# Kernel tuning notes

Hardware: AMD Instinct MI355X
Metric: run time of the kernel (lower is better)

The kernel has to match this reference:

```python
import jax, jax.numpy as jnp
import numpy as np

NUM_CHANNEL = 2                      # channels per telescope group
K = 7                                # hexagonal kernel size
N_LEV = [2048, 512, 128, 32, 8]      # pixels per level (stride-2 hex pooling ~ /4)
CHS = [2, 64, 128, 256, 512]         # channel progression n1->n_features->n2->n3->n4


def _iconv(x, idx, w, b):
    # x: [B,C,Nin], idx: [K,Nout], w: [O,C,K] -> [B,O,Nout]
    g = x[:, :, idx]                              # gather neighbours [B,C,K,Nout]
    return jnp.einsum('bckn,ock->bon', g, w) + b[None, :, None]


def _ipool(x, idx):
    # IndexedMaxPool2d: gather then max over kernel positions
    return x[:, :, idx].max(axis=2)               # [B,C,Nout]


def _bn(x, gamma, beta, eps=1e-5):
    # train-mode BatchNorm1d over (batch, pixel) dims, biased variance (torch semantics)
    m = x.mean(axis=(0, 2), keepdims=True)
    v = x.var(axis=(0, 2), keepdims=True)
    return (x - m) / jnp.sqrt(v + eps) * gamma[None, :, None] + beta[None, :, None]


def setup_inputs() -> dict:
    key = jax.random.key(0)
    ks = jax.random.split(key, 40)
    ki = iter(range(40))
    nk = lambda: ks[next(ki)]
    B = 256
    inp = {"x": jax.random.normal(nk(), (B, 2 * NUM_CHANNEL, N_LEV[0]), jnp.float32)}
    for i in range(4):
        inp[f"idx_conv{i+1}"] = jax.random.randint(nk(), (K, N_LEV[i]), 0, N_LEV[i])
        inp[f"idx_pool{i+1}"] = jax.random.randint(nk(), (K, N_LEV[i + 1]), 0, N_LEV[i])
        fan = float(CHS[i] * K)
        inp[f"w{i+1}"] = jax.random.normal(nk(), (CHS[i + 1], CHS[i], K), jnp.float32) / np.float32(np.sqrt(fan))
        inp[f"b{i+1}"] = jnp.zeros((CHS[i + 1],), jnp.float32)
        inp[f"gamma{i+1}"] = jnp.ones((CHS[i + 1],), jnp.float32)
        inp[f"beta{i+1}"] = jnp.zeros((CHS[i + 1],), jnp.float32)
    F = N_LEV[4] * CHS[4]            # 8 * 512 = 4096
    H = F // 2                       # 2048
    inp["lin1_w"] = jax.random.normal(nk(), (H, F), jnp.float32) / np.float32(np.sqrt(F))
    inp["lin1_b"] = jnp.zeros((H,), jnp.float32)
    inp["gamma5"] = jnp.ones((H,), jnp.float32)
    inp["beta5"] = jnp.zeros((H,), jnp.float32)
    inp["lin2_w"] = jax.random.normal(nk(), (3, H), jnp.float32) / np.float32(np.sqrt(H))
    inp["lin2_b"] = jnp.zeros((3,), jnp.float32)
    return inp


def reference(x, idx_conv1, idx_pool1, idx_conv2, idx_pool2, idx_conv3, idx_pool3,
              idx_conv4, idx_pool4, w1, b1, gamma1, beta1, w2, b2, gamma2, beta2,
              w3, b3, gamma3, beta3, w4, b4, gamma4, beta4,
              lin1_w, lin1_b, gamma5, beta5, lin2_w, lin2_b):
    layers = [(idx_conv1, idx_pool1, w1, b1, gamma1, beta1),
              (idx_conv2, idx_pool2, w2, b2, gamma2, beta2),
              (idx_conv3, idx_pool3, w3, b3, gamma3, beta3),
              (idx_conv4, idx_pool4, w4, b4, gamma4, beta4)]
    T = x.shape[1] // NUM_CHANNEL    # number of telescope groups (static)
    outs = []
    for i in range(T):
        o = x[:, i * NUM_CHANNEL:(i + 1) * NUM_CHANNEL, :]
        for (ic, ip, w, b, g, be) in layers:
            # conv -> pool -> bn -> relu (dropout with p=0 is identity)
            o = jax.nn.relu(_bn(_ipool(_iconv(o, ic, w, b), ip), g, be))
        outs.append(o)
    o = jnp.stack(outs, 1).mean(axis=1)          # [B, 512, 8]
    o = o.reshape(o.shape[0], -1)                # [B, 4096]
    o = o @ lin1_w.T + lin1_b                    # [B, 2048]
    m = o.mean(axis=0)
    v = o.var(axis=0)
    o = (o - m) / jnp.sqrt(v + 1e-5) * gamma5 + beta5
    o = jax.nn.relu(o)
    o = o @ lin2_w.T + lin2_b                    # [B, 3]
    cls = jax.nn.log_softmax(o[:, :2], axis=1)   # targets: class=2 (log-softmax), energy=1 (raw)
    return jnp.concatenate([cls, o[:, 2:3]], axis=1)
```

## Files before the change

kernel.cpp:

```cpp
#include <hip/hip_runtime.h>
#include <math.h>

#define B 256
#define KW 7

typedef __bf16 bf16x8 __attribute__((ext_vector_type(8)));
typedef __bf16 bf16x4 __attribute__((ext_vector_type(4)));
typedef float  f32x4  __attribute__((ext_vector_type(4)));

__device__ __forceinline__ void block_reduce2(float& s, float& s2, float* lds) {
    for (int off = 32; off > 0; off >>= 1) {
        s  += __shfl_down(s,  off, 64);
        s2 += __shfl_down(s2, off, 64);
    }
    int wave = threadIdx.x >> 6;
    int lane = threadIdx.x & 63;
    if (lane == 0) { lds[wave * 2] = s; lds[wave * 2 + 1] = s2; }
    __syncthreads();
    if (threadIdx.x == 0) {
        s  = lds[0] + lds[2] + lds[4] + lds[6];
        s2 = lds[1] + lds[3] + lds[5] + lds[7];
    }
}

__global__ __launch_bounds__(256) void k_transpose(const float* __restrict__ x,
                                                   float* __restrict__ A0) {
    int bid = blockIdx.x;
    int nt  = bid & 63;
    int rem = bid >> 6;
    int ci  = rem & 1;
    int t   = rem >> 1;
    int n0  = nt * 32;
    __shared__ float lds[32][257];
    int tid = threadIdx.x;
    int nl  = tid & 31;
    int bq  = tid >> 5;
    int ch  = t * 2 + ci;
    for (int p = 0; p < 32; p++) {
        int b = bq + p * 8;
        lds[nl][b] = x[((size_t)b * 4 + ch) * 2048 + n0 + nl];
    }
    __syncthreads();
    for (int nl2 = 0; nl2 < 32; nl2++) {
        A0[(((size_t)t * 2048 + n0 + nl2) * 2 + ci) * B + tid] = lds[nl2][tid];
    }
}

__global__ __launch_bounds__(256) void k_convpool1(
    const float* __restrict__ act,
    float* __restrict__ P1,
    const float* __restrict__ w,
    const float* __restrict__ bias,
    const int* __restrict__ idx_conv,
    const int* __restrict__ idx_pool,
    float* __restrict__ part1c)
{
    const int Kt = 14, C_out = 64, N_in = 2048, N_out = 512;
    int bid   = blockIdx.x;
    int cot   = bid & 1;
    int colid = bid >> 1;
    int t     = colid / N_out;
    int np    = colid - t * N_out;
    int co0   = cot << 5;

    __shared__ float lds_g[14 * 256];
    __shared__ float lds_w[14 * 33];
    __shared__ int   lds_idx[KW];

    int tid = threadIdx.x;
    int cog = tid >> 6;
    int bl  = tid & 63;

    float pmax[8][4];
    #pragma unroll
    for (int i = 0; i < 8; i++)
        #pragma unroll
        for (int j = 0; j < 4; j++) pmax[i][j] = -INFINITY;

    const float* actT = act + (size_t)t * N_in * 2 * B;

    for (int kp = 0; kp < KW; kp++) {
        int nc = idx_pool[kp * N_out + np];
        if (tid < KW) lds_idx[tid] = idx_conv[tid * N_in + nc];

        float acc[8][4];
        #pragma unroll
        for (int i = 0; i < 8; i++)
            #pragma unroll
            for (int j = 0; j < 4; j++) acc[i][j] = 0.f;

        __syncthreads();
        for (int e = tid; e < 32 * Kt; e += 256) {
            int kk = e % Kt;
            int co = e / Kt;
            lds_w[kk * 33 + co] = w[(size_t)(co0 + co) * Kt + kk];
        }
        for (int r = 0; r < Kt; r++) {
            int ci  = r / KW;
            int k   = r - ci * KW;
            int col = lds_idx[k];
            lds_g[r * 256 + tid] = actT[((size_t)col * 2 + ci) * B + tid];
        }
        __syncthreads();
        for (int kk = 0; kk < Kt; kk++) {
            float g0 = lds_g[kk * 256 + bl];
            float g1 = lds_g[kk * 256 + bl + 64];
            float g2 = lds_g[kk * 256 + bl + 128];
            float g3 = lds_g[kk * 256 + bl + 192];
            const float* wr = lds_w + kk * 33 + cog * 8;
            #pragma unroll
            for (int i = 0; i < 8; i++) {
                float wv = wr[i];
                acc[i][0] = fmaf(wv, g0, acc[i][0]);
                acc[i][1] = fmaf(wv, g1, acc[i][1]);
                acc[i][2] = fmaf(wv, g2, acc[i][2]);
                acc[i][3] = fmaf(wv, g3, acc[i][3]);
            }
        }
        #pragma unroll
        for (int i = 0; i < 8; i++)
            #pragma unroll
            for (int j = 0; j < 4; j++) pmax[i][j] = fmaxf(pmax[i][j], acc[i][j]);
    }

    float* outp = P1 + (((size_t)t * N_out + np) * C_out + co0) * B;
    float* pblk = part1c + (size_t)bid * 64;
    #pragma unroll
    for (int i = 0; i < 8; i++) {
        int co = cog * 8 + i;
        float bv = bias[co0 + co];
        float s = 0.f, s2 = 0.f;
        #pragma unroll
        for (int j = 0; j < 4; j++) {
            float val = pmax[i][j] + bv;
            outp[(size_t)co * B + bl + 64 * j] = val;
            s  += val;
            s2 += val * val;
        }
        for (int o = 32; o > 0; o >>= 1) {
            s  += __shfl_down(s,  o, 64);
            s2 += __shfl_down(s2, o, 64);
        }
        if ((tid & 63) == 0) {
            pblk[co]      = s;
            pblk[32 + co] = s2;
        }
    }
}

__global__ __launch_bounds__(256) void k_finstats1(
    const float* __restrict__ part1c,
    const float* __restrict__ gamma, const float* __restrict__ beta,
    float* __restrict__ scale, float* __restrict__ shift)
{
    int idx = blockIdx.x;
    int t = idx >> 6, c = idx & 63;
    int cot = c >> 5, cl = c & 31;
    float s = 0.f, s2 = 0.f;
    for (int np = threadIdx.x; np < 512; np += 256) {
        const float* pp = part1c + (size_t)((t * 512 + np) * 2 + cot) * 64;
        s  += pp[cl];
        s2 += pp[32 + cl];
    }
    __shared__ float lds[8];
    block_reduce2(s, s2, lds);
    if (threadIdx.x == 0) {
        float cnt  = 512.f * 256.f;
        float m    = s / cnt;
        float var  = s2 / cnt - m * m;
        float istd = rsqrtf(var + 1e-5f);
        float g    = gamma[c];
        scale[idx] = istd * g;
        shift[idx] = beta[c] - m * istd * g;
    }
}

__global__ __launch_bounds__(256) void k_bnrelu1t(
    const float* __restrict__ P1,
    const float* __restrict__ sc, const float* __restrict__ sh,
    __bf16* __restrict__ act1)
{
    int bid = blockIdx.x;
    int t = bid >> 9;
    int b = threadIdx.x;
    const float* src = P1 + (size_t)bid * 64 * B;
    __bf16* dst = act1 + (size_t)bid * B * 64 + (size_t)b * 64;
    const float* scp = sc + t * 64;
    const float* shp = sh + t * 64;
    __bf16 vals[64];
    #pragma unroll
    for (int co = 0; co < 64; co++) {
        float v = src[co * B + b];
        vals[co] = (__bf16)fmaxf(fmaf(v, scp[co], shp[co]), 0.f);
    }
    #pragma unroll
    for (int j = 0; j < 8; j++)
        *(bf16x8*)(dst + j * 8) = *(bf16x8*)&vals[j * 8];
}

__global__ void k_wr(const float* __restrict__ w, __bf16* __restrict__ wr,
                     int C_in, int total) {
    int idx = blockIdx.x * 256 + threadIdx.x;
    if (idx >= total) return;
    int ci = idx % C_in;
    int r  = idx / C_in;
    int kt = r % 7;
    int co = r / 7;
    wr[idx] = (__bf16)w[((size_t)co * C_in + ci) * 7 + kt];
}

__global__ void k_cvt8(const float* __restrict__ src, __bf16* __restrict__ dst, int total8) {
    int idx = blockIdx.x * 256 + threadIdx.x;
    if (idx >= total8) return;
    const f32x4* s4 = (const f32x4*)(src + (size_t)idx * 8);
    f32x4 a = s4[0], b = s4[1];
    bf16x8 v;
    v[0] = (__bf16)a[0]; v[1] = (__bf16)a[1]; v[2] = (__bf16)a[2]; v[3] = (__bf16)a[3];
    v[4] = (__bf16)b[0]; v[5] = (__bf16)b[1]; v[6] = (__bf16)b[2]; v[7] = (__bf16)b[3];
    *(bf16x8*)(dst + (size_t)idx * 8) = v;
}

__global__ __launch_bounds__(256) void k_conv_mfma(
    const __bf16* __restrict__ act,
    __bf16* __restrict__ convo,
    const __bf16* __restrict__ wr,
    const int* __restrict__ idx_conv,
    int C_in, int C_out, int N, int ci_shift)
{
    int nco = C_out >> 7;
    int bid = blockIdx.x;
    int cot = bid % nco;
    int rem = bid / nco;
    int n   = rem % N;
    int t   = rem / N;
    int co0 = cot * 128;
    int Kt  = C_in * KW;

    int tid  = threadIdx.x;
    int wv   = tid >> 6;
    int lane = tid & 63;
    int quad = lane >> 4;
    int lid  = lane & 15;

    f32x4 acc[8][4];
    #pragma unroll
    for (int i = 0; i < 8; i++)
        #pragma unroll
        for (int j = 0; j < 4; j++) {
            acc[i][j][0] = 0.f; acc[i][j][1] = 0.f;
            acc[i][j][2] = 0.f; acc[i][j][3] = 0.f;
        }

    const __bf16* actT = act + (size_t)t * N * B * C_in;
    const __bf16* wbase = wr + (size_t)(co0 + lid) * Kt + quad * 8;

    for (int k0 = 0; k0 < Kt; k0 += 32) {
        int kt  = k0 >> ci_shift;
        int ci0 = k0 & (C_in - 1);
        int col = idx_conv[kt * N + n];

        bf16x8 bfrag[4];
        const __bf16* gbase = actT + ((size_t)col * B + wv * 64 + lid) * C_in + ci0 + quad * 8;
        #pragma unroll
        for (int bt = 0; bt < 4; bt++)
            bfrag[bt] = *(const bf16x8*)(gbase + (size_t)bt * 16 * C_in);

        #pragma unroll
        for (int rt = 0; rt < 8; rt++) {
            bf16x8 afrag = *(const bf16x8*)(wbase + (size_t)rt * 16 * Kt + k0);
            #pragma unroll
            for (int bt = 0; bt < 4; bt++)
                acc[rt][bt] = __builtin_amdgcn_mfma_f32_16x16x32_bf16(
                    afrag, bfrag[bt], acc[rt][bt], 0, 0, 0);
        }
    }

    __bf16* outp = convo + ((size_t)(t * N + n) * B) * C_out;
    #pragma unroll
    for (int rt = 0; rt < 8; rt++)
        #pragma unroll
        for (int bt = 0; bt < 4; bt++) {
            int b  = wv * 64 + bt * 16 + lid;
            int co = co0 + rt * 16 + quad * 4;
            bf16x4 v;
            v[0] = (__bf16)acc[rt][bt][0];
            v[1] = (__bf16)acc[rt][bt][1];
            v[2] = (__bf16)acc[rt][bt][2];
            v[3] = (__bf16)acc[rt][bt][3];
            *(bf16x4*)(outp + (size_t)b * C_out + co) = v;
        }
}

__global__ __launch_bounds__(256) void k_poolstats(
    const __bf16* __restrict__ convo,
    float* __restrict__ P,
    const float* __restrict__ bias,
    const int* __restrict__ idx_pool,
    float* __restrict__ part,
    int C, int N, int No)
{
    int bid  = blockIdx.x;
    int bg   = bid & 3;
    int rem  = bid >> 2;
    int np   = rem % No;
    int t    = rem / No;
    int cols[7];
    #pragma unroll
    for (int k = 0; k < 7; k++) cols[k] = idx_pool[k * No + np];
    const __bf16* base = convo + (size_t)t * N * B * C;
    float* pout = P + ((size_t)(t * No + np) * B) * C;
    int tid = threadIdx.x;
    float s[2] = {0.f, 0.f}, s2[2] = {0.f, 0.f};
    int NC, c0, bstart, bstep, nb;
    if (C >= 256) { NC = C >> 8; c0 = tid;           bstart = 0;        bstep = 1; nb = 64; }
    else          { NC = 1;      c0 = tid & (C - 1); bstart = tid >> 7; bstep = 2; nb = 32; }
    for (int j = 0; j < NC; j++) {
        int c = c0 + j * 256;
        float bv = bias[c];
        for (int i = 0; i < nb; i++) {
            int b = bg * 64 + bstart + i * bstep;
            float m = -1e30f;
            #pragma unroll
            for (int k = 0; k < 7; k++) {
                float v = (float)base[((size_t)cols[k] * B + b) * C + c];
                m = fmaxf(m, v);
            }
            float val = m + bv;
            pout[(size_t)b * C + c] = val;
            s[j] += val; s2[j] += val * val;
        }
    }
    float* pp = part + (size_t)((t * No + np) * 4 + bg) * 1024;
    for (int j = 0; j < NC; j++) {
        pp[tid + j * 256]       = s[j];
        pp[512 + tid + j * 256] = s2[j];
    }
}

__global__ __launch_bounds__(256) void k_finstats(
    const float* __restrict__ part,
    const float* __restrict__ gamma, const float* __restrict__ beta,
    float* __restrict__ scale, float* __restrict__ shift,
    int C, int No)
{
    int idx = blockIdx.x;
    int t = idx / C, c = idx - t * C;
    int SMAX   = C < 256 ? 256 : C;
    int nslice = SMAX / C;
    int nblk   = No * 4;
    int total  = nblk * nslice;
    const float* pbase = part + (size_t)(t * No * 4) * 1024;
    float s = 0.f, s2 = 0.f;
    for (int e = threadIdx.x; e < total; e += 256) {
        int blk = e / nslice;
        int j   = e - blk * nslice;
        const float* pp = pbase + (size_t)blk * 1024;
        int sl = c + j * C;
        s  += pp[sl];
        s2 += pp[512 + sl];
    }
    __shared__ float lds[8];
    block_reduce2(s, s2, lds);
    if (threadIdx.x == 0) {
        float cnt  = (float)No * 256.f;
        float m    = s / cnt;
        float var  = s2 / cnt - m * m;
        float istd = rsqrtf(var + 1e-5f);
        float g    = gamma[c];
        scale[idx] = istd * g;
        shift[idx] = beta[c] - m * istd * g;
    }
}

__global__ void k_bnrelu(const float* __restrict__ P, __bf16* __restrict__ act,
                         const float* __restrict__ scale, const float* __restrict__ shift,
                         int C, int total)
{
    int idx = blockIdx.x * 256 + threadIdx.x;
    if (idx >= total) return;
    int c = idx & (C - 1);
    int t = idx >= (total >> 1) ? 1 : 0;
    int tc = t * C + c;
    float v = P[idx];
    act[idx] = (__bf16)fmaxf(fmaf(v, scale[tc], shift[tc]), 0.f);
}

__global__ __launch_bounds__(256) void k_zbuild(const float* __restrict__ P4,
                                                const float* __restrict__ sc4,
                                                const float* __restrict__ sh4,
                                                __bf16* __restrict__ z)
{
    int b = blockIdx.x;
    int tid = threadIdx.x;
    for (int j = 0; j < 2; j++) {
        int c = tid + j * 256;
        float s0 = sc4[c],       h0 = sh4[c];
        float s1 = sc4[512 + c], h1 = sh4[512 + c];
        #pragma unroll
        for (int np = 0; np < 8; np++) {
            float v0 = P4[(((size_t)0 * 8 + np) * B + b) * 512 + c];
            float v1 = P4[(((size_t)1 * 8 + np) * B + b) * 512 + c];
            float y0 = fmaxf(fmaf(v0, s0, h0), 0.f);
            float y1 = fmaxf(fmaf(v1, s1, h1), 0.f);
            z[(size_t)b * 4096 + c * 8 + np] = (__bf16)(0.5f * (y0 + y1));
        }
    }
}

__global__ __launch_bounds__(256) void k_lin1_part(
    const __bf16* __restrict__ zb,
    const __bf16* __restrict__ w1b,
    float* __restrict__ partL)
{
    int ht = blockIdx.x >> 3;
    int ks = blockIdx.x & 7;
    int h0 = ht * 64;
    int f_beg = ks * 512, f_end = f_beg + 512;

    int tid  = threadIdx.x;
    int wv   = tid >> 6;
    int lane = tid & 63;
    int quad = lane >> 4;
    int lid  = lane & 15;

    f32x4 acc[4][4];
    #pragma unroll
    for (int i = 0; i < 4; i++)
        #pragma unroll
        for (int j = 0; j < 4; j++) {
            acc[i][j][0] = 0.f; acc[i][j][1] = 0.f;
            acc[i][j][2] = 0.f; acc[i][j][3] = 0.f;
        }

    const __bf16* wbase = w1b + (size_t)(h0 + lid) * 4096 + quad * 8;
    const __bf16* zbase = zb + ((size_t)(wv * 64 + lid)) * 4096 + quad * 8;

    for (int f0 = f_beg; f0 < f_end; f0 += 32) {
        bf16x8 afrag[4];
        #pragma unroll
        for (int rt = 0; rt < 4; rt++)
            afrag[rt] = *(const bf16x8*)(wbase + (size_t)rt * 16 * 4096 + f0);
        bf16x8 bfrag[4];
        #pragma unroll
        for (int bt = 0; bt < 4; bt++)
            bfrag[bt] = *(const bf16x8*)(zbase + (size_t)bt * 16 * 4096 + f0);
        #pragma unroll
        for (int rt = 0; rt < 4; rt++)
            #pragma unroll
            for (int bt = 0; bt < 4; bt++)
                acc[rt][bt] = __builtin_amdgcn_mfma_f32_16x16x32_bf16(
                    afrag[rt], bfrag[bt], acc[rt][bt], 0, 0, 0);
    }
    float* outp = partL + (size_t)ks * 2048 * B;
    #pragma unroll
    for (int rt = 0; rt < 4; rt++)
        #pragma unroll
        for (int bt = 0; bt < 4; bt++) {
            int b = wv * 64 + bt * 16 + lid;
            int h = h0 + rt * 16 + quad * 4;
            #pragma unroll
            for (int r = 0; r < 4; r++)
                outp[(size_t)(h + r) * B + b] = acc[rt][bt][r];
        }
}

__global__ __launch_bounds__(256) void k_redstats5(
    const float* __restrict__ partL,
    const float* __restrict__ b1,
    const float* __restrict__ gamma5, const float* __restrict__ beta5,
    float* __restrict__ o1,
    float* __restrict__ scale5, float* __restrict__ shift5)
{
    int h = blockIdx.x;
    int b = threadIdx.x;
    float v = b1[h];
    #pragma unroll
    for (int s = 0; s < 8; s++)
        v += partL[((size_t)s * 2048 + h) * B + b];
    o1[(size_t)h * B + b] = v;
    float s1 = v, s2 = v * v;
    __shared__ float lds[8];
    block_reduce2(s1, s2, lds);
    if (threadIdx.x == 0) {
        float m    = s1 * (1.f / 256.f);
        float var  = s2 * (1.f / 256.f) - m * m;
        float istd = rsqrtf(var + 1e-5f);
        float g    = gamma5[h];
        scale5[h]  = istd * g;
        shift5[h]  = beta5[h] - m * istd * g;
    }
}

__global__ __launch_bounds__(256) void k_final(
    const float* __restrict__ o1,
    const float* __restrict__ scale5, const float* __restrict__ shift5,
    const float* __restrict__ w2, const float* __restrict__ b2,
    float* __restrict__ out)
{
    int b = blockIdx.x;
    int tid = threadIdx.x;
    float s0 = 0.f, s1 = 0.f, s2v = 0.f;
    for (int h = tid; h < 2048; h += 256) {
        float y = fmaxf(fmaf(o1[(size_t)h * B + b], scale5[h], shift5[h]), 0.f);
        s0  = fmaf(y, w2[h],        s0);
        s1  = fmaf(y, w2[2048 + h], s1);
        s2v = fmaf(y, w2[4096 + h], s2v);
    }
    for (int off = 32; off > 0; off >>= 1) {
        s0  += __shfl_down(s0,  off, 64);
        s1  += __shfl_down(s1,  off, 64);
        s2v += __shfl_down(s2v, off, 64);
    }
    __shared__ float lds[12];
    int wave = tid >> 6, lane = tid & 63;
    if (lane == 0) { lds[wave * 3] = s0; lds[wave * 3 + 1] = s1; lds[wave * 3 + 2] = s2v; }
    __syncthreads();
    if (tid == 0) {
        float o0 = lds[0] + lds[3] + lds[6] + lds[9]  + b2[0];
        float oa = lds[1] + lds[4] + lds[7] + lds[10] + b2[1];
        float ob = lds[2] + lds[5] + lds[8] + lds[11] + b2[2];
        float m   = fmaxf(o0, oa);
        float lse = m + logf(expf(o0 - m) + expf(oa - m));
        out[b * 3 + 0] = o0 - lse;
        out[b * 3 + 1] = oa - lse;
        out[b * 3 + 2] = ob;
    }
}

extern "C" void kernel_launch(void* const* d_in, const int* in_sizes, int n_in,
                              void* d_out, int out_size, void* d_ws, size_t ws_size,
                              hipStream_t stream) {
    (void)in_sizes; (void)n_in; (void)out_size; (void)ws_size;

    const float* x   = (const float*)d_in[0];
    const int*   ic1 = (const int*)d_in[1];
    const int*   ip1 = (const int*)d_in[2];
    const float* pW1 = (const float*)d_in[3];
    const float* pB1 = (const float*)d_in[4];
    const float* pG1 = (const float*)d_in[5];
    const float* pE1 = (const float*)d_in[6];
    const int*   ic2 = (const int*)d_in[7];
    const int*   ip2 = (const int*)d_in[8];
    const float* pW2 = (const float*)d_in[9];
    const float* pB2 = (const float*)d_in[10];
    const float* pG2 = (const float*)d_in[11];
    const float* pE2 = (const float*)d_in[12];
    const int*   ic3 = (const int*)d_in[13];
    const int*   ip3 = (const int*)d_in[14];
    const float* pW3 = (const float*)d_in[15];
    const float* pB3 = (const float*)d_in[16];
    const float* pG3 = (const float*)d_in[17];
    const float* pE3 = (const float*)d_in[18];
    const int*   ic4 = (const int*)d_in[19];
    const int*   ip4 = (const int*)d_in[20];
    const float* pW4 = (const float*)d_in[21];
    const float* pB4 = (const float*)d_in[22];
    const float* pG4 = (const float*)d_in[23];
    const float* pE4 = (const float*)d_in[24];
    const float* lw1 = (const float*)d_in[25];
    const float* lb1 = (const float*)d_in[26];
    const float* g5  = (const float*)d_in[27];
    const float* e5  = (const float*)d_in[28];
    const float* lw2 = (const float*)d_in[29];
    const float* lb2 = (const float*)d_in[30];

    char* ws = (char*)d_ws;
    size_t off = 0;
    auto alloc = [&](size_t bytes) -> char* {
        char* p = ws + off;
        off += (bytes + 511) & ~(size_t)511;
        return p;
    };

    float*  A0    = (float*) alloc((size_t)2 * 2048 * 2 * B * 4);
    __bf16* act1  = (__bf16*)alloc((size_t)2 * 512 * B * 64 * 2);
    char*   U     =          alloc((size_t)512 * B * 128 * 4);
    float*  P1f   = (float*)U;
    __bf16* convX = (__bf16*)U;
    float*  partL = (float*)U;
    float*  Pf    = (float*) alloc((size_t)2 * 128 * B * 128 * 4);
    __bf16* actS  = (__bf16*)alloc((size_t)2 * 128 * B * 128 * 2);
    __bf16* Wr2   = (__bf16*)alloc((size_t)128 * 448 * 2);
    __bf16* Wr3   = (__bf16*)alloc((size_t)256 * 896 * 2);
    __bf16* Wr4   = (__bf16*)alloc((size_t)512 * 1792 * 2);
    __bf16* w1b   = (__bf16*)alloc((size_t)2048 * 4096 * 2);
    __bf16* z     = (__bf16*)alloc((size_t)256 * 4096 * 2);
    float*  o1    = (float*) alloc((size_t)2048 * B * 4);
    float*  part  = (float*) alloc((size_t)2 * 128 * 4 * 1024 * 4);
    float*  part1c= (float*) alloc((size_t)2048 * 64 * 4);
    float*  sc1 = (float*)alloc(2 * 64 * 4);
    float*  sh1 = (float*)alloc(2 * 64 * 4);
    float*  sc2 = (float*)alloc(2 * 128 * 4);
    float*  sh2 = (float*)alloc(2 * 128 * 4);
    float*  sc3 = (float*)alloc(2 * 256 * 4);
    float*  sh3 = (float*)alloc(2 * 256 * 4);
    float*  sc4 = (float*)alloc(2 * 512 * 4);
    float*  sh4 = (float*)alloc(2 * 512 * 4);
    float*  sc5 = (float*)alloc(2048 * 4);
    float*  sh5 = (float*)alloc(2048 * 4);

    k_wr<<<(128 * 448 + 255) / 256, 256, 0, stream>>>(pW2, Wr2, 64, 128 * 448);
    k_wr<<<(256 * 896 + 255) / 256, 256, 0, stream>>>(pW3, Wr3, 128, 256 * 896);
    k_wr<<<(512 * 1792 + 255) / 256, 256, 0, stream>>>(pW4, Wr4, 256, 512 * 1792);
    k_cvt8<<<(2048 * 4096 / 8) / 256, 256, 0, stream>>>(lw1, w1b, 2048 * 4096 / 8);

    k_transpose<<<256, 256, 0, stream>>>(x, A0);

    k_convpool1<<<2048, 256, 0, stream>>>(A0, P1f, pW1, pB1, ic1, ip1, part1c);
    k_finstats1<<<2 * 64, 256, 0, stream>>>(part1c, pG1, pE1, sc1, sh1);
    k_bnrelu1t<<<2 * 512, 256, 0, stream>>>(P1f, sc1, sh1, act1);

    k_conv_mfma<<<1 * 512 * 2, 256, 0, stream>>>(act1, convX, Wr2, ic2, 64, 128, 512, 6);
    k_poolstats<<<2 * 128 * 4, 256, 0, stream>>>(convX, Pf, pB2, ip2, part, 128, 512, 128);
    k_finstats<<<2 * 128, 256, 0, stream>>>(part, pG2, pE2, sc2, sh2, 128, 128);
    k_bnrelu<<<(2 * 128 * B * 128) / 256, 256, 0, stream>>>(Pf, actS, sc2, sh2, 128, 2 * 128 * B * 128);

    k_conv_mfma<<<2 * 128 * 2, 256, 0, stream>>>(actS, convX, Wr3, ic3, 128, 256, 128, 7);
    k_poolstats<<<2 * 32 * 4, 256, 0, stream>>>(convX, Pf, pB3, ip3, part, 256, 128, 32);
    k_finstats<<<2 * 256, 256, 0, stream>>>(part, pG3, pE3, sc3, sh3, 256, 32);
    k_bnrelu<<<(2 * 32 * B * 256) / 256, 256, 0, stream>>>(Pf, actS, sc3, sh3, 256, 2 * 32 * B * 256);

    k_conv_mfma<<<4 * 32 * 2, 256, 0, stream>>>(actS, convX, Wr4, ic4, 256, 512, 32, 8);
    k_poolstats<<<2 * 8 * 4, 256, 0, stream>>>(convX, Pf, pB4, ip4, part, 512, 32, 8);
    k_finstats<<<2 * 512, 256, 0, stream>>>(part, pG4, pE4, sc4, sh4, 512, 8);

    k_zbuild<<<256, 256, 0, stream>>>(Pf, sc4, sh4, z);
    k_lin1_part<<<256, 256, 0, stream>>>(z, w1b, partL);
    k_redstats5<<<2048, 256, 0, stream>>>(partL, lb1, g5, e5, o1, sc5, sh5);
    k_final<<<256, 256, 0, stream>>>(o1, sc5, sh5, lw2, lb2, (float*)d_out);
}
```

Measured before the change: 702.9 us.

## Fuse weight-prep kernels and double-buffer gathered B fragments in MFMA conv

Merges the three weight-reorder launches and the lin1 bf16 conversion into a single prep kernel, which removes launch overhead. In the MFMA conv kernel, all seven gather indices are loaded into registers once up front, and the next K-slice's activation fragments are prefetched while the current slice's MFMAs run. This hides gather latency at the cost of more VGPRs, which may lower occupancy.

```diff
diff --git a/kernel.cpp b/kernel.cpp
--- a/kernel.cpp
+++ b/kernel.cpp
@@ -198,26 +198,40 @@
         *(bf16x8*)(dst + j * 8) = *(bf16x8*)&vals[j * 8];
 }
 
-__global__ void k_wr(const float* __restrict__ w, __bf16* __restrict__ wr,
-                     int C_in, int total) {
+__global__ __launch_bounds__(256) void k_prep(
+    const float* __restrict__ w2, const float* __restrict__ w3,
+    const float* __restrict__ w4, const float* __restrict__ lw1,
+    __bf16* __restrict__ Wr2, __bf16* __restrict__ Wr3,
+    __bf16* __restrict__ Wr4, __bf16* __restrict__ w1b)
+{
+    const int n2 = 128 * 448, n3 = 256 * 896, n4 = 512 * 1792, n1 = (2048 * 4096) / 8;
     int idx = blockIdx.x * 256 + threadIdx.x;
-    if (idx >= total) return;
-    int ci = idx % C_in;
-    int r  = idx / C_in;
-    int kt = r % 7;
-    int co = r / 7;
-    wr[idx] = (__bf16)w[((size_t)co * C_in + ci) * 7 + kt];
-}
-
-__global__ void k_cvt8(const float* __restrict__ src, __bf16* __restrict__ dst, int total8) {
-    int idx = blockIdx.x * 256 + threadIdx.x;
-    if (idx >= total8) return;
-    const f32x4* s4 = (const f32x4*)(src + (size_t)idx * 8);
-    f32x4 a = s4[0], b = s4[1];
-    bf16x8 v;
-    v[0] = (__bf16)a[0]; v[1] = (__bf16)a[1]; v[2] = (__bf16)a[2]; v[3] = (__bf16)a[3];
-    v[4] = (__bf16)b[0]; v[5] = (__bf16)b[1]; v[6] = (__bf16)b[2]; v[7] = (__bf16)b[3];
-    *(bf16x8*)(dst + (size_t)idx * 8) = v;
+    if (idx < n2) {
+        int ci = idx & 63; int r = idx >> 6; int kt = r % 7; int co = r / 7;
+        Wr2[idx] = (__bf16)w2[((size_t)co * 64 + ci) * 7 + kt];
+        return;
+    }
+    idx -= n2;
+    if (idx < n3) {
+        int ci = idx & 127; int r = idx >> 7; int kt = r % 7; int co = r / 7;
+        Wr3[idx] = (__bf16)w3[((size_t)co * 128 + ci) * 7 + kt];
+        return;
+    }
+    idx -= n3;
+    if (idx < n4) {
+        int ci = idx & 255; int r = idx >> 8; int kt = r % 7; int co = r / 7;
+        Wr4[idx] = (__bf16)w4[((size_t)co * 256 + ci) * 7 + kt];
+        return;
+    }
+    idx -= n4;
+    if (idx < n1) {
+        const f32x4* s4 = (const f32x4*)(lw1 + (size_t)idx * 8);
+        f32x4 a = s4[0], b = s4[1];
+        bf16x8 v;
+        v[0] = (__bf16)a[0]; v[1] = (__bf16)a[1]; v[2] = (__bf16)a[2]; v[3] = (__bf16)a[3];
+        v[4] = (__bf16)b[0]; v[5] = (__bf16)b[1]; v[6] = (__bf16)b[2]; v[7] = (__bf16)b[3];
+        *(bf16x8*)(w1b + (size_t)idx * 8) = v;
+    }
 }
 
 __global__ __launch_bounds__(256) void k_conv_mfma(
@@ -242,6 +256,10 @@
     int quad = lane >> 4;
     int lid  = lane & 15;
 
+    int cols[KW];
+    #pragma unroll
+    for (int k = 0; k < KW; k++) cols[k] = idx_conv[k * N + n];
+
     f32x4 acc[8][4];
     #pragma unroll
     for (int i = 0; i < 8; i++)
@@ -251,28 +269,41 @@
             acc[i][j][2] = 0.f; acc[i][j][3] = 0.f;
         }
 
-    const __bf16* actT = act + (size_t)t * N * B * C_in;
+    const __bf16* actT  = act + (size_t)t * N * B * C_in
+                              + ((size_t)(wv * 64 + lid)) * C_in + quad * 8;
     const __bf16* wbase = wr + (size_t)(co0 + lid) * Kt + quad * 8;
 
-    for (int k0 = 0; k0 < Kt; k0 += 32) {
-        int kt  = k0 >> ci_shift;
-        int ci0 = k0 & (C_in - 1);
-        int col = idx_conv[kt * N + n];
-
-        bf16x8 bfrag[4];
-        const __bf16* gbase = actT + ((size_t)col * B + wv * 64 + lid) * C_in + ci0 + quad * 8;
+    int niter = Kt >> 5;
+
+    bf16x8 bcur[4], bnxt[4];
+    {
+        const __bf16* g = actT + (size_t)cols[0] * B * C_in;
         #pragma unroll
         for (int bt = 0; bt < 4; bt++)
-            bfrag[bt] = *(const bf16x8*)(gbase + (size_t)bt * 16 * C_in);
-
+            bcur[bt] = *(const bf16x8*)(g + (size_t)bt * 16 * C_in);
+    }
+
+    for (int it = 0; it < niter; it++) {
+        int k0 = it << 5;
+        if (it + 1 < niter) {
+            int k1  = k0 + 32;
+            int kt  = k1 >> ci_shift;
+            int ci0 = k1 & (C_in - 1);
+            const __bf16* g = actT + (size_t)cols[kt] * B * C_in + ci0;
+            #pragma unroll
+            for (int bt = 0; bt < 4; bt++)
+                bnxt[bt] = *(const bf16x8*)(g + (size_t)bt * 16 * C_in);
+        }
         #pragma unroll
         for (int rt = 0; rt < 8; rt++) {
             bf16x8 afrag = *(const bf16x8*)(wbase + (size_t)rt * 16 * Kt + k0);
             #pragma unroll
             for (int bt = 0; bt < 4; bt++)
                 acc[rt][bt] = __builtin_amdgcn_mfma_f32_16x16x32_bf16(
-                    afrag, bfrag[bt], acc[rt][bt], 0, 0, 0);
-        }
+                    afrag, bcur[bt], acc[rt][bt], 0, 0, 0);
+        }
+        #pragma unroll
+        for (int bt = 0; bt < 4; bt++) bcur[bt] = bnxt[bt];
     }
 
     __bf16* outp = convo + ((size_t)(t * N + n) * B) * C_out;
@@ -599,10 +630,11 @@
     float*  sc5 = (float*)alloc(2048 * 4);
     float*  sh5 = (float*)alloc(2048 * 4);
 
-    k_wr<<<(128 * 448 + 255) / 256, 256, 0, stream>>>(pW2, Wr2, 64, 128 * 448);
-    k_wr<<<(256 * 896 + 255) / 256, 256, 0, stream>>>(pW3, Wr3, 128, 256 * 896);
-    k_wr<<<(512 * 1792 + 255) / 256, 256, 0, stream>>>(pW4, Wr4, 256, 512 * 1792);
-    k_cvt8<<<(2048 * 4096 / 8) / 256, 256, 0, stream>>>(lw1, w1b, 2048 * 4096 / 8);
+    {
+        const int total = 128 * 448 + 256 * 896 + 512 * 1792 + (2048 * 4096) / 8;
+        k_prep<<<(total + 255) / 256, 256, 0, stream>>>(pW2, pW3, pW4, lw1,
+                                                        Wr2, Wr3, Wr4, w1b);
+    }
 
     k_transpose<<<256, 256, 0, stream>>>(x, A0);
 
```

After: 713.5 us. About the same (+1.5%).
